# Kernel tuning notes

Hardware: AMD Instinct MI355X
Metric: run time of the kernel (lower is better)

Reference implementation:

```python
import jax, jax.numpy as jnp
import numpy as np

IN_FEATURES = 1024
OUT_FEATURES = 1024
THRESHOLD = 0.05


def ternary_quantize(x, threshold):
    # {-1, 0, +1}: zero where |x| < threshold, else sign(x)
    return jnp.where(jnp.abs(x) < threshold, jnp.zeros_like(x), jnp.sign(x))


def setup_inputs() -> dict:
    key = jax.random.key(0)
    kx, kw = jax.random.split(key)
    x = jax.random.normal(kx, (32768, IN_FEATURES), dtype=jnp.float32)
    # xavier_uniform for weight [out, in]: bound = sqrt(6/(fan_in+fan_out))
    bound = float(np.sqrt(6.0 / (IN_FEATURES + OUT_FEATURES)))
    weight = jax.random.uniform(kw, (OUT_FEATURES, IN_FEATURES), dtype=jnp.float32,
                                minval=-bound, maxval=bound)
    return {"x": x, "weight": weight}


def reference(x, weight):
    x_tern = ternary_quantize(x, THRESHOLD).astype(jnp.int8)
    w_tern = ternary_quantize(weight, THRESHOLD).astype(jnp.int8)
    # int32 accumulate matmul: [T, in] @ [in, out] -> [T, out]
    out = jnp.matmul(x_tern.astype(jnp.int32), w_tern.astype(jnp.int32).T)
    return out.astype(jnp.float32)
```

## Files before the change

### kernel.cpp

```cpp
#include <hip/hip_runtime.h>

#define THRESH 0.05f

typedef __attribute__((ext_vector_type(4)))  int   int32x4;
typedef __attribute__((ext_vector_type(16))) int   int32x16;
typedef __attribute__((ext_vector_type(4)))  float floatx4;

__global__ __launch_bounds__(256) void quant_w_kernel(const float* __restrict__ w,
                                                      signed char* __restrict__ wqf) {
    int c = blockIdx.x * 256 + threadIdx.x;
    int l  = c & 63;
    int k  = (c >> 6) & 31;
    int nb = c >> 11;
    int col   = nb * 32 + (l & 31);
    int kbase = k * 32 + (l >> 5) * 16;
    const float* src = w + col * 1024 + kbase;
    signed char q[16];
    #pragma unroll
    for (int j = 0; j < 4; ++j) {
        float4 f = *(const float4*)(src + j * 4);
        q[j * 4 + 0] = (signed char)((f.x >= THRESH) - (f.x <= -THRESH));
        q[j * 4 + 1] = (signed char)((f.y >= THRESH) - (f.y <= -THRESH));
        q[j * 4 + 2] = (signed char)((f.z >= THRESH) - (f.z <= -THRESH));
        q[j * 4 + 3] = (signed char)((f.w >= THRESH) - (f.w <= -THRESH));
    }
    *(int32x4*)(wqf + (size_t)c * 16) = *(const int32x4*)q;
}

__global__ __launch_bounds__(512, 4) void tern_gemm_kernel(const float* __restrict__ x,
                                                           const signed char* __restrict__ wqf,
                                                           float* __restrict__ out) {
    __shared__ __attribute__((aligned(16))) signed char a_lds[64 * 1024];
    const int tid = threadIdx.x;
    const long rowbase = (long)blockIdx.x * 64;

    #pragma unroll
    for (int i = 0; i < 8; ++i) {
        int c   = tid + i * 512;
        int row = c >> 6;
        int cir = c & 63;
        const floatx4* src = (const floatx4*)(x + (rowbase + row) * 1024 + cir * 16);
        signed char q[16];
        #pragma unroll
        for (int j = 0; j < 4; ++j) {
            floatx4 f = __builtin_nontemporal_load(src + j);
            #pragma unroll
            for (int e = 0; e < 4; ++e)
                q[j * 4 + e] = (signed char)((f[e] >= THRESH) - (f[e] <= -THRESH));
        }
        int k    = cir >> 1;
        int blk  = k * 2 + (row >> 5);
        int slot = ((cir & 1) * 32 + (row & 31)) ^ (k & 7);
        *(int32x4*)(a_lds + blk * 1024 + slot * 16) = *(const int32x4*)q;
    }
    __syncthreads();

    const int wave = tid >> 6;
    const int lane = tid & 63;
    const int l31  = lane & 31;
    const int hi   = lane >> 5;

    for (int ot = 0; ot < 4; ++ot) {
        const int nb = ot * 8 + wave;
        const signed char* bp = wqf + (size_t)nb * 32768 + lane * 16;

        int32x16 acc0 = {0,0,0,0,0,0,0,0,0,0,0,0,0,0,0,0};
        int32x16 acc1 = acc0;

        #pragma unroll
        for (int ks = 0; ks < 4; ++ks) {
            int32x4 b[8];
            #pragma unroll
            for (int j = 0; j < 8; ++j)
                b[j] = *(const int32x4*)(bp + (size_t)(ks * 8 + j) * 1024);
            __builtin_amdgcn_sched_barrier(0);
            #pragma unroll
            for (int j = 0; j < 8; ++j) {
                const int k  = ks * 8 + j;
                const int sl = (lane ^ (k & 7)) * 16;
                int32x4 af0 = *(const int32x4*)(a_lds + (k * 2 + 0) * 1024 + sl);
                int32x4 af1 = *(const int32x4*)(a_lds + (k * 2 + 1) * 1024 + sl);
                acc0 = __builtin_amdgcn_mfma_i32_32x32x32_i8(af0, b[j], acc0, 0, 0, 0);
                acc1 = __builtin_amdgcn_mfma_i32_32x32x32_i8(af1, b[j], acc1, 0, 0, 0);
            }
        }

        const int cb = nb * 32 + l31;
        #pragma unroll
        for (int r = 0; r < 16; ++r) {
            const int rit = (r & 3) + 8 * (r >> 2) + 4 * hi;
            float* o0 = out + (rowbase + rit) * 1024 + cb;
            float* o1 = o0 + 32L * 1024;
            __builtin_nontemporal_store((float)acc0[r], o0);
            __builtin_nontemporal_store((float)acc1[r], o1);
        }
    }
}

extern "C" void kernel_launch(void* const* d_in, const int* in_sizes, int n_in,
                              void* d_out, int out_size, void* d_ws, size_t ws_size,
                              hipStream_t stream) {
    const float* x = (const float*)d_in[0];
    const float* w = (const float*)d_in[1];
    float* out = (float*)d_out;
    signed char* wqf = (signed char*)d_ws;

    quant_w_kernel<<<dim3(256), dim3(256), 0, stream>>>(w, wqf);
    tern_gemm_kernel<<<dim3(512), dim3(512), 0, stream>>>(x, wqf, out);
}
```

Baseline: 265.5 us.

## Double-buffer weight fragment loads to overlap global reads with MFMA

Replaces the load-8-then-compute loop with a two-buffer software pipeline: the next 4 weight fragments are fetched from global memory while the MFMAs consume the current 4, and the first fetch for each output tile is issued during the previous tile. The initial weight load is also issued before the LDS barrier so it overlaps the activation quantization. The aim is to hide global-load latency behind matrix work. The cost is more live registers for two buffers, which may pressure occupancy, and the final iteration issues a redundant prefetch that is never used.

```diff
diff --git a/kernel.cpp b/kernel.cpp
--- a/kernel.cpp
+++ b/kernel.cpp
@@ -27,6 +27,25 @@
     *(int32x4*)(wqf + (size_t)c * 16) = *(const int32x4*)q;
 }
 
+#define LOADB(buf, base_ptr, kb) do {                                          \
+    _Pragma("unroll")                                                          \
+    for (int j = 0; j < 4; ++j)                                                \
+        buf[j] = *(const int32x4*)((base_ptr) + (size_t)((kb) + j) * 1024);    \
+    __builtin_amdgcn_sched_barrier(0);                                         \
+} while (0)
+
+#define COMPB(buf, kb) do {                                                    \
+    _Pragma("unroll")                                                          \
+    for (int j = 0; j < 4; ++j) {                                              \
+        const int k_  = (kb) + j;                                              \
+        const int sl_ = (lane ^ (k_ & 7)) * 16;                                \
+        int32x4 af0 = *(const int32x4*)(a_lds + (k_ * 2 + 0) * 1024 + sl_);    \
+        int32x4 af1 = *(const int32x4*)(a_lds + (k_ * 2 + 1) * 1024 + sl_);    \
+        acc0 = __builtin_amdgcn_mfma_i32_32x32x32_i8(af0, buf[j], acc0, 0, 0, 0); \
+        acc1 = __builtin_amdgcn_mfma_i32_32x32x32_i8(af1, buf[j], acc1, 0, 0, 0); \
+    }                                                                          \
+} while (0)
+
 __global__ __launch_bounds__(512, 4) void tern_gemm_kernel(const float* __restrict__ x,
                                                            const signed char* __restrict__ wqf,
                                                            float* __restrict__ out) {
@@ -53,37 +72,35 @@
         int slot = ((cir & 1) * 32 + (row & 31)) ^ (k & 7);
         *(int32x4*)(a_lds + blk * 1024 + slot * 16) = *(const int32x4*)q;
     }
-    __syncthreads();
 
     const int wave = tid >> 6;
     const int lane = tid & 63;
     const int l31  = lane & 31;
     const int hi   = lane >> 5;
 
+    const signed char* bp0 = wqf + (size_t)wave * 32768 + lane * 16;
+
+    int32x4 bA[4], bB[4];
+    LOADB(bA, bp0, 0);
+
+    __syncthreads();
+
     for (int ot = 0; ot < 4; ++ot) {
+        const signed char* bp  = bp0 + (size_t)ot * 8 * 32768;
+        const signed char* bpn = (ot == 3) ? bp0 : bp + 8 * 32768;
         const int nb = ot * 8 + wave;
-        const signed char* bp = wqf + (size_t)nb * 32768 + lane * 16;
 
         int32x16 acc0 = {0,0,0,0,0,0,0,0,0,0,0,0,0,0,0,0};
         int32x16 acc1 = acc0;
 
-        #pragma unroll
-        for (int ks = 0; ks < 4; ++ks) {
-            int32x4 b[8];
-            #pragma unroll
-            for (int j = 0; j < 8; ++j)
-                b[j] = *(const int32x4*)(bp + (size_t)(ks * 8 + j) * 1024);
-            __builtin_amdgcn_sched_barrier(0);
-            #pragma unroll
-            for (int j = 0; j < 8; ++j) {
-                const int k  = ks * 8 + j;
-                const int sl = (lane ^ (k & 7)) * 16;
-                int32x4 af0 = *(const int32x4*)(a_lds + (k * 2 + 0) * 1024 + sl);
-                int32x4 af1 = *(const int32x4*)(a_lds + (k * 2 + 1) * 1024 + sl);
-                acc0 = __builtin_amdgcn_mfma_i32_32x32x32_i8(af0, b[j], acc0, 0, 0, 0);
-                acc1 = __builtin_amdgcn_mfma_i32_32x32x32_i8(af1, b[j], acc1, 0, 0, 0);
-            }
-        }
+        LOADB(bB, bp, 4);    COMPB(bA, 0);
+        LOADB(bA, bp, 8);    COMPB(bB, 4);
+        LOADB(bB, bp, 12);   COMPB(bA, 8);
+        LOADB(bA, bp, 16);   COMPB(bB, 12);
+        LOADB(bB, bp, 20);   COMPB(bA, 16);
+        LOADB(bA, bp, 24);   COMPB(bB, 20);
+        LOADB(bB, bp, 28);   COMPB(bA, 24);
+        LOADB(bA, bpn, 0);   COMPB(bB, 28);
 
         const int cb = nb * 32 + l31;
         #pragma unroll
```

New measurement: 276.7 us. 1.04x slower.

## Pre-quantize x to int8 in workspace and split GEMM across column blocks

Applied to the files above, without the earlier changes.

Adds a separate kernel that quantizes x into an MFMA-fragment-ordered int8 buffer in workspace. A new GEMM kernel tiles 64 rows by 256 columns per block across 2048 blocks and streams the A operand through a double-buffered LDS ring, overlapping loads with MFMAs. The aim is to raise parallelism and cut LDS footprint compared with the old one-block-per-64-rows design. The cost is an extra int8 write and read of x (32 MB) plus per-chunk barriers. It falls back to the old kernel when the workspace is too small.

```diff
diff --git a/kernel.cpp b/kernel.cpp
--- a/kernel.cpp
+++ b/kernel.cpp
@@ -27,9 +27,99 @@
     *(int32x4*)(wqf + (size_t)c * 16) = *(const int32x4*)q;
 }
 
-__global__ __launch_bounds__(512, 4) void tern_gemm_kernel(const float* __restrict__ x,
-                                                           const signed char* __restrict__ wqf,
-                                                           float* __restrict__ out) {
+__global__ __launch_bounds__(256) void quant_x_kernel(const float* __restrict__ x,
+                                                      signed char* __restrict__ xq) {
+    int c = blockIdx.x * 256 + threadIdx.x;
+    int l  = c & 63;
+    int k  = (c >> 6) & 31;
+    int mb = c >> 11;
+    long row  = (long)mb * 32 + (l & 31);
+    int kbase = k * 32 + (l >> 5) * 16;
+    const float* src = x + row * 1024 + kbase;
+    signed char q[16];
+    #pragma unroll
+    for (int j = 0; j < 4; ++j) {
+        float4 f = *(const float4*)(src + j * 4);
+        q[j * 4 + 0] = (signed char)((f.x >= THRESH) - (f.x <= -THRESH));
+        q[j * 4 + 1] = (signed char)((f.y >= THRESH) - (f.y <= -THRESH));
+        q[j * 4 + 2] = (signed char)((f.z >= THRESH) - (f.z <= -THRESH));
+        q[j * 4 + 3] = (signed char)((f.w >= THRESH) - (f.w <= -THRESH));
+    }
+    *(int32x4*)(xq + (size_t)c * 16) = *(const int32x4*)q;
+}
+
+__global__ __launch_bounds__(512, 4) void tern_gemm_v2(const signed char* __restrict__ xq,
+                                                       const signed char* __restrict__ wqf,
+                                                       float* __restrict__ out) {
+    __shared__ __attribute__((aligned(16))) signed char a_lds[2][8192];
+    const int tid  = threadIdx.x;
+    const int wv   = tid >> 6;
+    const int lane = tid & 63;
+    const int l31  = lane & 31;
+    const int hi   = lane >> 5;
+
+    const int rb = blockIdx.x >> 2;
+    const int cb = blockIdx.x & 3;
+    const long rowbase = (long)rb * 64;
+
+    const int mbloc = wv & 1;
+    const int kloc  = wv >> 1;
+    const int mb    = rb * 2 + mbloc;
+    const signed char* xsrc = xq + ((size_t)(mb * 32 + kloc) * 64 + lane) * 16;
+    signed char* ldst = &a_lds[0][0] + (kloc * 2 + mbloc) * 1024 + lane * 16;
+
+    const int nb = cb * 8 + wv;
+    const signed char* bp = wqf + (size_t)nb * 32768 + lane * 16;
+
+    int32x16 acc0 = {0,0,0,0,0,0,0,0,0,0,0,0,0,0,0,0};
+    int32x16 acc1 = acc0;
+
+    {
+        int32x4 x0 = *(const int32x4*)xsrc;
+        *(int32x4*)ldst = x0;
+    }
+    __syncthreads();
+
+    #pragma unroll
+    for (int c = 0; c < 8; ++c) {
+        const int bi = c & 1;
+        const signed char* lb = &a_lds[bi][0];
+
+        int32x4 b0 = *(const int32x4*)(bp + (size_t)(c * 4 + 0) * 1024);
+        int32x4 b1 = *(const int32x4*)(bp + (size_t)(c * 4 + 1) * 1024);
+        int32x4 b2 = *(const int32x4*)(bp + (size_t)(c * 4 + 2) * 1024);
+        int32x4 b3 = *(const int32x4*)(bp + (size_t)(c * 4 + 3) * 1024);
+        int32x4 xn = {0, 0, 0, 0};
+        if (c < 7) xn = *(const int32x4*)(xsrc + (size_t)(c + 1) * 4096);
+        __builtin_amdgcn_sched_barrier(0);
+
+        #pragma unroll
+        for (int j = 0; j < 4; ++j) {
+            const int32x4 bj = (j == 0) ? b0 : (j == 1) ? b1 : (j == 2) ? b2 : b3;
+            int32x4 af0 = *(const int32x4*)(lb + (j * 2 + 0) * 1024 + lane * 16);
+            int32x4 af1 = *(const int32x4*)(lb + (j * 2 + 1) * 1024 + lane * 16);
+            acc0 = __builtin_amdgcn_mfma_i32_32x32x32_i8(af0, bj, acc0, 0, 0, 0);
+            acc1 = __builtin_amdgcn_mfma_i32_32x32x32_i8(af1, bj, acc1, 0, 0, 0);
+        }
+
+        if (c < 7) *(int32x4*)(ldst + (bi ^ 1) * 8192) = xn;
+        __syncthreads();
+    }
+
+    const int ccol = nb * 32 + l31;
+    #pragma unroll
+    for (int r = 0; r < 16; ++r) {
+        const int rit = (r & 3) + 8 * (r >> 2) + 4 * hi;
+        float* o0 = out + (rowbase + rit) * 1024 + ccol;
+        float* o1 = o0 + 32L * 1024;
+        __builtin_nontemporal_store((float)acc0[r], o0);
+        __builtin_nontemporal_store((float)acc1[r], o1);
+    }
+}
+
+__global__ __launch_bounds__(512, 4) void tern_gemm_fb(const float* __restrict__ x,
+                                                       const signed char* __restrict__ wqf,
+                                                       float* __restrict__ out) {
     __shared__ __attribute__((aligned(16))) signed char a_lds[64 * 1024];
     const int tid = threadIdx.x;
     const long rowbase = (long)blockIdx.x * 64;
@@ -85,11 +175,11 @@
             }
         }
 
-        const int cb = nb * 32 + l31;
+        const int cbcol = nb * 32 + l31;
         #pragma unroll
         for (int r = 0; r < 16; ++r) {
             const int rit = (r & 3) + 8 * (r >> 2) + 4 * hi;
-            float* o0 = out + (rowbase + rit) * 1024 + cb;
+            float* o0 = out + (rowbase + rit) * 1024 + cbcol;
             float* o1 = o0 + 32L * 1024;
             __builtin_nontemporal_store((float)acc0[r], o0);
             __builtin_nontemporal_store((float)acc1[r], o1);
@@ -104,7 +194,14 @@
     const float* w = (const float*)d_in[1];
     float* out = (float*)d_out;
     signed char* wqf = (signed char*)d_ws;
+    signed char* xq  = (signed char*)d_ws + (1u << 20);
 
     quant_w_kernel<<<dim3(256), dim3(256), 0, stream>>>(w, wqf);
-    tern_gemm_kernel<<<dim3(512), dim3(512), 0, stream>>>(x, wqf, out);
-}
+
+    if (ws_size >= 33ull * 1024 * 1024) {
+        quant_x_kernel<<<dim3(8192), dim3(256), 0, stream>>>(x, xq);
+        tern_gemm_v2<<<dim3(2048), dim3(512), 0, stream>>>(xq, wqf, out);
+    } else {
+        tern_gemm_fb<<<dim3(512), dim3(512), 0, stream>>>(x, wqf, out);
+    }
+}
```

Measured after the change: 270.3 us. No clear change (+1.8%).
